# Optimization experiments

Hardware: AMD Instinct MI355X
Metric: run time of the kernel (lower is better)

Reference implementation:

```python
import jax, jax.numpy as jnp
import numpy as np

N_NODES = 100000
N_EDGES = 800000
IN_DIM, HID_DIM, OUT_DIM = 128, 256, 40


def setup_inputs() -> dict:
    key = jax.random.key(0)
    ks = jax.random.split(key, 8)
    x = jax.random.normal(ks[0], (N_NODES, IN_DIM), dtype=jnp.float32)
    edge_index = jax.random.randint(ks[1], (2, N_EDGES), 0, N_NODES, dtype=jnp.int64)
    # PyG SAGEConv params: lin_l (neighbor path, with bias), lin_r (root path, no bias)
    def glorot(k, fan_in, fan_out):
        lim = np.sqrt(6.0 / (fan_in + fan_out)).astype(np.float32)
        return jax.random.uniform(k, (fan_in, fan_out), jnp.float32, -lim, lim)
    W1l = glorot(ks[2], IN_DIM, HID_DIM)
    W1r = glorot(ks[3], IN_DIM, HID_DIM)
    b1 = jnp.zeros((HID_DIM,), jnp.float32)
    W2l = glorot(ks[4], HID_DIM, OUT_DIM)
    W2r = glorot(ks[5], HID_DIM, OUT_DIM)
    b2 = jnp.zeros((OUT_DIM,), jnp.float32)
    return {"x": x, "edge_index": edge_index, "W1l": W1l, "b1": b1, "W1r": W1r,
            "W2l": W2l, "b2": b2, "W2r": W2r}


def _sage_conv(x, src, dst, Wl, b, Wr, n_nodes):
    # mean aggregation of neighbor features: gather x[src], scatter-add to dst, divide by degree
    msg = x[src]                                              # [E, D]
    agg = jax.ops.segment_sum(msg, dst, num_segments=n_nodes)  # [N, D]
    cnt = jax.ops.segment_sum(jnp.ones((src.shape[0],), x.dtype), dst,
                              num_segments=n_nodes)            # [N]
    agg = agg / jnp.maximum(cnt, 1.0)[:, None]
    # out = lin_l(mean_agg) + lin_r(x)  (lin_l carries the bias in PyG)
    return agg @ Wl + b + x @ Wr


def reference(x, edge_index, W1l, b1, W1r, W2l, b2, W2r):
    src, dst = edge_index[0], edge_index[1]
    n = x.shape[0]
    h = _sage_conv(x, src, dst, W1l, b1, W1r, n)
    h = jax.nn.relu(h)
    # F.dropout(training=self.training): identity at inference
    out = _sage_conv(h, src, dst, W2l, b2, W2r, n)
    return out
```

## Files before the change

kernel.cpp:

```cpp
#include <hip/hip_runtime.h>
#include <hip/hip_bf16.h>


#define NN   100000
#define NNP  100096
#define NE   800000
#define NB1  391

typedef unsigned short ushortT;
typedef __attribute__((ext_vector_type(8))) short bf16x8;
typedef __attribute__((ext_vector_type(4))) float f32x4;

__device__ __forceinline__ unsigned short f2b(float f) {
    unsigned u = __float_as_uint(f);
    return (unsigned short)((u + 0x7fffu + ((u >> 16) & 1u)) >> 16);
}
__device__ __forceinline__ float b2f(unsigned short v) {
    return __uint_as_float(((unsigned)v) << 16);
}
__device__ __forceinline__ void llds16(const unsigned short* g, unsigned short* s) {
    __builtin_amdgcn_global_load_lds(
        (const __attribute__((address_space(1))) void*)g,
        (__attribute__((address_space(3))) void*)s, 16, 0, 0);
}

__global__ __launch_bounds__(256) void k_rank(const int* __restrict__ dst,
                                              int* __restrict__ deg,
                                              int* __restrict__ rank) {
    int e = blockIdx.x * 256 + threadIdx.x;
    if (e < NE) rank[e] = atomicAdd(&deg[dst[e]], 1);
}

__global__ __launch_bounds__(256) void k_scan1(const int* __restrict__ deg,
                                               int* __restrict__ rp,
                                               int* __restrict__ bsum) {
    __shared__ int s[256];
    int t = threadIdx.x;
    int i = blockIdx.x * 256 + t;
    int v = (i < NN) ? deg[i] : 0;
    s[t] = v;
    __syncthreads();
    for (int off = 1; off < 256; off <<= 1) {
        int add = (t >= off) ? s[t - off] : 0;
        __syncthreads();
        s[t] += add;
        __syncthreads();
    }
    if (i < NN) rp[i] = s[t] - v;
    if (t == 255) bsum[blockIdx.x] = s[255];
}

__global__ __launch_bounds__(512) void k_scan2(int* __restrict__ bsum) {
    __shared__ int s[512];
    int t = threadIdx.x;
    int v = (t < NB1) ? bsum[t] : 0;
    s[t] = v;
    __syncthreads();
    for (int off = 1; off < 512; off <<= 1) {
        int add = (t >= off) ? s[t - off] : 0;
        __syncthreads();
        s[t] += add;
        __syncthreads();
    }
    if (t < NB1) bsum[t] = s[t] - v;
}

__global__ __launch_bounds__(256) void k_scan3(int* __restrict__ rp,
                                               const int* __restrict__ bsum) {
    int i = blockIdx.x * 256 + threadIdx.x;
    if (i < NN) rp[i] += bsum[blockIdx.x];
    if (i == 0) rp[NN] = NE;
}

__global__ __launch_bounds__(256) void k_fill(const int* __restrict__ src,
                                              const int* __restrict__ dst,
                                              const int* __restrict__ rank,
                                              const int* __restrict__ rp,
                                              int* __restrict__ col) {
    int e = blockIdx.x * 256 + threadIdx.x;
    if (e < NE) col[rp[dst[e]] + rank[e]] = src[e];
}

__global__ __launch_bounds__(256) void k_prep(const float* __restrict__ x,
                                              const float* __restrict__ W1l,
                                              const float* __restrict__ W1r,
                                              const float* __restrict__ W2l,
                                              const float* __restrict__ W2r,
                                              ushortT* __restrict__ Ac,
                                              ushortT* __restrict__ WT1,
                                              ushortT* __restrict__ WT2,
                                              int* __restrict__ deg) {
    int t = blockIdx.x * 256 + threadIdx.x;
    int row = t >> 5, c4 = t & 31;
    float4 v = *(const float4*)&x[(size_t)row * 128 + c4 * 4];
    ushortT* p = Ac + (size_t)row * 256 + 128 + c4 * 4;
    p[0] = f2b(v.x); p[1] = f2b(v.y); p[2] = f2b(v.z); p[3] = f2b(v.w);

    if (t < NN) deg[t] = 0;
    if (t < 65536) {
        int n = t >> 8, k = t & 255;
        float w = (k < 128) ? W1l[(size_t)k * 256 + n] : W1r[(size_t)(k - 128) * 256 + n];
        WT1[t] = f2b(w);
    } else if (t < 65536 + 20480) {
        int j = t - 65536;
        int n = j >> 8, k = j & 255;
        float w = (n < 40) ? W2l[(size_t)k * 40 + n] : W2r[(size_t)k * 40 + (n - 40)];
        WT2[j] = f2b(w);
    }
}

__global__ __launch_bounds__(256) void k_agg1(const int* __restrict__ rp,
                                              const int* __restrict__ col,
                                              ushortT* __restrict__ Ac) {
    int node = blockIdx.x * 4 + (threadIdx.x >> 6);
    int l = threadIdx.x & 63;
    if (node >= NN) return;
    int seg = l >> 4, dl = l & 15;
    int beg = rp[node];
    int deg = rp[node + 1] - beg;
    float a[8] = {0.f, 0.f, 0.f, 0.f, 0.f, 0.f, 0.f, 0.f};
    for (int base = 0; base < deg; base += 64) {
        int cnt = min(64, deg - base);
        int cv = col[beg + base + min(l, cnt - 1)];
        for (int j = 0; j < cnt; j += 8) {
            int e0 = j + seg, e1 = j + 4 + seg;
            int i0 = __shfl(cv, min(e0, cnt - 1));
            int i1 = __shfl(cv, min(e1, cnt - 1));
            bf16x8 v0 = {0, 0, 0, 0, 0, 0, 0, 0};
            bf16x8 v1 = {0, 0, 0, 0, 0, 0, 0, 0};
            if (e0 < cnt) v0 = *(const bf16x8*)(Ac + (size_t)i0 * 256 + 128 + dl * 8);
            if (e1 < cnt) v1 = *(const bf16x8*)(Ac + (size_t)i1 * 256 + 128 + dl * 8);
#pragma unroll
            for (int i = 0; i < 8; ++i)
                a[i] += b2f((unsigned short)v0[i]) + b2f((unsigned short)v1[i]);
        }
    }
#pragma unroll
    for (int i = 0; i < 8; ++i) {
        a[i] += __shfl_xor(a[i], 16);
        a[i] += __shfl_xor(a[i], 32);
    }
    if (seg == 0) {
        float inv = 1.0f / fmaxf((float)deg, 1.0f);
        bf16x8 o;
#pragma unroll
        for (int i = 0; i < 8; ++i) o[i] = (short)f2b(a[i] * inv);
        *(bf16x8*)(Ac + (size_t)node * 256 + dl * 8) = o;
    }
}

__global__ __launch_bounds__(256, 4) void k_gemm1(const ushortT* __restrict__ Ac,
                                                  const ushortT* __restrict__ WT1,
                                                  const float* __restrict__ b1,
                                                  ushortT* __restrict__ h) {
    __shared__ ushortT As[128 * 64];
    __shared__ ushortT Bs[128 * 64];
    const int tid = threadIdx.x, l = tid & 63, wid = tid >> 6;
    const int wm = wid & 1, wn = wid >> 1;
    const int m0 = blockIdx.x * 128;
    const int n0 = blockIdx.y * 128;
    const int q = l >> 4, r = l & 15;
    const int swz = (l & 7) ^ ((l >> 3) & 7);

    f32x4 acc[4][4];
#pragma unroll
    for (int i = 0; i < 4; ++i)
#pragma unroll
        for (int j = 0; j < 4; ++j) acc[i][j] = (f32x4){0.f, 0.f, 0.f, 0.f};

    for (int kt = 0; kt < 256; kt += 64) {
#pragma unroll
        for (int i = 0; i < 4; ++i) {
            int flat = wid * 4 + i;
            int row = flat * 8 + (l >> 3);
            llds16(Ac + (size_t)(m0 + row) * 256 + kt + swz * 8, &As[flat * 512]);
        }
#pragma unroll
        for (int i = 0; i < 4; ++i) {
            int flat = wid * 4 + i;
            int row = flat * 8 + (l >> 3);
            llds16(WT1 + (size_t)(n0 + row) * 256 + kt + swz * 8, &Bs[flat * 512]);
        }
        __syncthreads();
#pragma unroll
        for (int ks = 0; ks < 64; ks += 32) {
            bf16x8 af[4], bfr[4];
            const int c0 = (ks >> 3) + q;
            const int cs = (c0 ^ (r & 7)) * 8;
#pragma unroll
            for (int mt = 0; mt < 4; ++mt)
                af[mt] = *(const bf16x8*)&As[(wm * 64 + mt * 16 + r) * 64 + cs];
#pragma unroll
            for (int nt = 0; nt < 4; ++nt)
                bfr[nt] = *(const bf16x8*)&Bs[(wn * 64 + nt * 16 + r) * 64 + cs];
#pragma unroll
            for (int mt = 0; mt < 4; ++mt)
#pragma unroll
                for (int nt = 0; nt < 4; ++nt)
                    acc[mt][nt] = __builtin_amdgcn_mfma_f32_16x16x32_bf16(
                        af[mt], bfr[nt], acc[mt][nt], 0, 0, 0);
        }
        __syncthreads();
    }
#pragma unroll
    for (int mt = 0; mt < 4; ++mt) {
        int row0 = m0 + wm * 64 + mt * 16 + q * 4;
#pragma unroll
        for (int nt = 0; nt < 4; ++nt) {
            int colb = n0 + wn * 64 + nt * 16 + r;
            float bb = b1[colb];
#pragma unroll
            for (int j = 0; j < 4; ++j) {
                float v = fmaxf(acc[mt][nt][j] + bb, 0.f);
                h[(size_t)(row0 + j) * 256 + colb] = f2b(v);
            }
        }
    }
}

__global__ __launch_bounds__(256, 4) void k_gemm2(const ushortT* __restrict__ h,
                                                  const ushortT* __restrict__ WT2,
                                                  const float* __restrict__ b2,
                                                  ushortT* __restrict__ y2,
                                                  float* __restrict__ t) {
    __shared__ ushortT As[128 * 64];
    __shared__ ushortT Bs[80 * 64];
    const int tid = threadIdx.x, l = tid & 63, wid = tid >> 6;
    const int m0 = blockIdx.x * 128;
    const int q = l >> 4, r = l & 15;
    const int swz = (l & 7) ^ ((l >> 3) & 7);

    f32x4 acc[2][5];
#pragma unroll
    for (int i = 0; i < 2; ++i)
#pragma unroll
        for (int j = 0; j < 5; ++j) acc[i][j] = (f32x4){0.f, 0.f, 0.f, 0.f};

    for (int kt = 0; kt < 256; kt += 64) {
#pragma unroll
        for (int i = 0; i < 4; ++i) {
            int flat = wid * 4 + i;
            int row = flat * 8 + (l >> 3);
            llds16(h + (size_t)(m0 + row) * 256 + kt + swz * 8, &As[flat * 512]);
        }
#pragma unroll
        for (int i = 0; i < 3; ++i) {
            int flat = wid * 3 + i;
            if (flat < 10) {
                int row = flat * 8 + (l >> 3);
                llds16(WT2 + (size_t)row * 256 + kt + swz * 8, &Bs[flat * 512]);
            }
        }
        __syncthreads();
#pragma unroll
        for (int ks = 0; ks < 64; ks += 32) {
            bf16x8 af[2], bfr[5];
            const int c0 = (ks >> 3) + q;
            const int cs = (c0 ^ (r & 7)) * 8;
#pragma unroll
            for (int mt = 0; mt < 2; ++mt)
                af[mt] = *(const bf16x8*)&As[(wid * 32 + mt * 16 + r) * 64 + cs];
#pragma unroll
            for (int nt = 0; nt < 5; ++nt)
                bfr[nt] = *(const bf16x8*)&Bs[(nt * 16 + r) * 64 + cs];
#pragma unroll
            for (int mt = 0; mt < 2; ++mt)
#pragma unroll
                for (int nt = 0; nt < 5; ++nt)
                    acc[mt][nt] = __builtin_amdgcn_mfma_f32_16x16x32_bf16(
                        af[mt], bfr[nt], acc[mt][nt], 0, 0, 0);
        }
        __syncthreads();
    }
#pragma unroll
    for (int mt = 0; mt < 2; ++mt) {
        int row0 = m0 + wid * 32 + mt * 16 + q * 4;
#pragma unroll
        for (int nt = 0; nt < 5; ++nt) {
            int c = nt * 16 + r;
            float bb = (c >= 40) ? b2[c - 40] : 0.f;
#pragma unroll
            for (int j = 0; j < 4; ++j) {
                float v = acc[mt][nt][j];
                if (c < 40)
                    y2[(size_t)(row0 + j) * 40 + c] = f2b(v);
                else
                    t[(size_t)(row0 + j) * 40 + (c - 40)] = v + bb;
            }
        }
    }
}

__global__ __launch_bounds__(256) void k_agg2(const int* __restrict__ rp,
                                              const int* __restrict__ col,
                                              const ushortT* __restrict__ y2,
                                              const float* __restrict__ t,
                                              float* __restrict__ out) {
    int node = blockIdx.x * 4 + (threadIdx.x >> 6);
    int l = threadIdx.x & 63;
    if (node >= NN) return;
    int seg = l >> 4, dl = l & 15;
    int beg = rp[node];
    int deg = rp[node + 1] - beg;
    bool act = dl < 10;
    float a0 = 0.f, a1 = 0.f, a2 = 0.f, a3 = 0.f;
    for (int base = 0; base < deg; base += 64) {
        int cnt = min(64, deg - base);
        int cv = col[beg + base + min(l, cnt - 1)];
        for (int j = 0; j < cnt; j += 8) {
            int e0 = j + seg, e1 = j + 4 + seg;
            int i0 = __shfl(cv, min(e0, cnt - 1));
            int i1 = __shfl(cv, min(e1, cnt - 1));
            ushort4 v0 = {0, 0, 0, 0}, v1 = {0, 0, 0, 0};
            if (e0 < cnt && act) v0 = *(const ushort4*)(y2 + (size_t)i0 * 40 + dl * 4);
            if (e1 < cnt && act) v1 = *(const ushort4*)(y2 + (size_t)i1 * 40 + dl * 4);
            a0 += b2f(v0.x) + b2f(v1.x);
            a1 += b2f(v0.y) + b2f(v1.y);
            a2 += b2f(v0.z) + b2f(v1.z);
            a3 += b2f(v0.w) + b2f(v1.w);
        }
    }
    a0 += __shfl_xor(a0, 16); a0 += __shfl_xor(a0, 32);
    a1 += __shfl_xor(a1, 16); a1 += __shfl_xor(a1, 32);
    a2 += __shfl_xor(a2, 16); a2 += __shfl_xor(a2, 32);
    a3 += __shfl_xor(a3, 16); a3 += __shfl_xor(a3, 32);
    if (seg == 0 && act) {
        float inv = 1.0f / fmaxf((float)deg, 1.0f);
        size_t o = (size_t)node * 40 + dl * 4;
        float4 tv = *(const float4*)&t[o];
        float4 ov;
        ov.x = a0 * inv + tv.x;
        ov.y = a1 * inv + tv.y;
        ov.z = a2 * inv + tv.z;
        ov.w = a3 * inv + tv.w;
        *(float4*)&out[o] = ov;
    }
}

extern "C" void kernel_launch(void* const* d_in, const int* in_sizes, int n_in,
                              void* d_out, int out_size, void* d_ws, size_t ws_size,
                              hipStream_t stream) {
    const float* x   = (const float*)d_in[0];
    const int*   ei  = (const int*)d_in[1];
    const int*   src = ei;
    const int*   dst = ei + NE;
    const float* W1l = (const float*)d_in[2];
    const float* b1  = (const float*)d_in[3];
    const float* W1r = (const float*)d_in[4];
    const float* W2l = (const float*)d_in[5];
    const float* b2  = (const float*)d_in[6];
    const float* W2r = (const float*)d_in[7];
    float* out = (float*)d_out;

    size_t off = 0;
    char* base = (char*)d_ws;
    auto alloc = [&](size_t bytes) -> void* {
        void* p = base + off;
        off += (bytes + 255) & ~(size_t)255;
        return p;
    };
    int*     deg  = (int*)alloc((size_t)NN * 4);
    int*     rp   = (int*)alloc((size_t)(NN + 1) * 4);
    int*     rank = (int*)alloc((size_t)NE * 4);
    int*     bsum = (int*)alloc(512 * 4);
    int*     col  = (int*)alloc((size_t)NE * 4);
    ushortT* Ac   = (ushortT*)alloc((size_t)NNP * 256 * 2);
    ushortT* h    = (ushortT*)alloc((size_t)NNP * 256 * 2);
    ushortT* y2   = (ushortT*)alloc((size_t)NNP * 40 * 2);
    float*   t    = (float*)alloc((size_t)NNP * 40 * 4);
    ushortT* WT1  = (ushortT*)alloc(256 * 256 * 2);
    ushortT* WT2  = (ushortT*)alloc(80 * 256 * 2);

    k_prep<<<(NN * 32) / 256, 256, 0, stream>>>(x, W1l, W1r, W2l, W2r, Ac, WT1, WT2, deg);
    k_rank<<<(NE + 255) / 256, 256, 0, stream>>>(dst, deg, rank);
    k_scan1<<<NB1, 256, 0, stream>>>(deg, rp, bsum);
    k_scan2<<<1, 512, 0, stream>>>(bsum);
    k_scan3<<<NB1, 256, 0, stream>>>(rp, bsum);
    k_fill<<<(NE + 255) / 256, 256, 0, stream>>>(src, dst, rank, rp, col);

    k_agg1<<<(NN + 3) / 4, 256, 0, stream>>>(rp, col, Ac);
    k_gemm1<<<dim3(NNP / 128, 2), 256, 0, stream>>>(Ac, WT1, b1, h);
    k_gemm2<<<NNP / 128, 256, 0, stream>>>(h, WT2, b2, y2, t);
    k_agg2<<<(NN + 3) / 4, 256, 0, stream>>>(rp, col, y2, t, out);
}
```

Baseline: 287.9 us.

## Fuse GEMM1 and GEMM2 via LDS, merge prep/rank, single-pass lookback scan

Fuses the two dense GEMMs into one kernel. Each block computes a 64-row tile of the hidden layer across all 256 columns, keeps the ReLU'd bf16 result in LDS, and multiplies it by WT2 straight away, so the hidden tensor is never written to or read back from global memory. It also merges the prep and rank kernels into one launch, zeroes deg with a memset, and swaps the three-kernel scan for a decoupled-lookback single-pass scan. Risks: each fused block reloads the full WT1 tile, the larger LDS footprint caps occupancy, and the lookback spin-wait assumes earlier blocks get scheduled, which costs time if they are delayed.

```diff
diff --git a/kernel.cpp b/kernel.cpp
--- a/kernel.cpp
+++ b/kernel.cpp
@@ -24,19 +24,50 @@
         (__attribute__((address_space(3))) void*)s, 16, 0, 0);
 }
 
-__global__ __launch_bounds__(256) void k_rank(const int* __restrict__ dst,
-                                              int* __restrict__ deg,
-                                              int* __restrict__ rank) {
-    int e = blockIdx.x * 256 + threadIdx.x;
-    if (e < NE) rank[e] = atomicAdd(&deg[dst[e]], 1);
-}
-
-__global__ __launch_bounds__(256) void k_scan1(const int* __restrict__ deg,
-                                               int* __restrict__ rp,
-                                               int* __restrict__ bsum) {
+__global__ __launch_bounds__(256) void k_prep_rank(
+        const float* __restrict__ x,
+        const float* __restrict__ W1l, const float* __restrict__ W1r,
+        const float* __restrict__ W2l, const float* __restrict__ W2r,
+        ushortT* __restrict__ Ac, ushortT* __restrict__ WT1,
+        ushortT* __restrict__ WT2, int* __restrict__ stat,
+        const int* __restrict__ dst, int* __restrict__ deg,
+        int* __restrict__ rank) {
+    int bid = blockIdx.x;
+    if (bid < 12500) {
+        int t = bid * 256 + threadIdx.x;
+        int row = t >> 5, c4 = t & 31;
+        float4 v = *(const float4*)&x[(size_t)row * 128 + c4 * 4];
+        ushortT* p = Ac + (size_t)row * 256 + 128 + c4 * 4;
+        p[0] = f2b(v.x); p[1] = f2b(v.y); p[2] = f2b(v.z); p[3] = f2b(v.w);
+
+        if (t < 512) stat[t] = 0;
+        if (t < 65536) {
+            int n = t >> 8, k = t & 255;
+            float w = (k < 128) ? W1l[(size_t)k * 256 + n]
+                                : W1r[(size_t)(k - 128) * 256 + n];
+            WT1[t] = f2b(w);
+        } else if (t < 65536 + 20480) {
+            int j = t - 65536;
+            int n = j >> 8, k = j & 255;
+            float w = (n < 40) ? W2l[(size_t)k * 40 + n]
+                               : W2r[(size_t)k * 40 + (n - 40)];
+            WT2[j] = f2b(w);
+        }
+    } else {
+        int e = (bid - 12500) * 256 + threadIdx.x;
+        if (e < NE) rank[e] = atomicAdd(&deg[dst[e]], 1);
+    }
+}
+
+__global__ __launch_bounds__(256) void k_scan(const int* __restrict__ deg,
+                                              int* __restrict__ rp,
+                                              int* __restrict__ aggv,
+                                              int* __restrict__ prefv,
+                                              int* __restrict__ stat) {
     __shared__ int s[256];
-    int t = threadIdx.x;
-    int i = blockIdx.x * 256 + t;
+    __shared__ int sprefix;
+    int t = threadIdx.x, b = blockIdx.x;
+    int i = b * 256 + t;
     int v = (i < NN) ? deg[i] : 0;
     s[t] = v;
     __syncthreads();
@@ -46,30 +77,36 @@
         s[t] += add;
         __syncthreads();
     }
-    if (i < NN) rp[i] = s[t] - v;
-    if (t == 255) bsum[blockIdx.x] = s[255];
-}
-
-__global__ __launch_bounds__(512) void k_scan2(int* __restrict__ bsum) {
-    __shared__ int s[512];
-    int t = threadIdx.x;
-    int v = (t < NB1) ? bsum[t] : 0;
-    s[t] = v;
+    int total = s[255];
+    if (t == 0) {
+        if (b == 0) {
+            __hip_atomic_store(&prefv[0], total, __ATOMIC_RELEASE, __HIP_MEMORY_SCOPE_AGENT);
+            __hip_atomic_store(&stat[0], 2, __ATOMIC_RELEASE, __HIP_MEMORY_SCOPE_AGENT);
+            sprefix = 0;
+        } else {
+            __hip_atomic_store(&aggv[b], total, __ATOMIC_RELEASE, __HIP_MEMORY_SCOPE_AGENT);
+            __hip_atomic_store(&stat[b], 1, __ATOMIC_RELEASE, __HIP_MEMORY_SCOPE_AGENT);
+            int run = 0, j = b - 1;
+            while (true) {
+                int sj;
+                do {
+                    sj = __hip_atomic_load(&stat[j], __ATOMIC_ACQUIRE, __HIP_MEMORY_SCOPE_AGENT);
+                } while (sj == 0);
+                if (sj == 2) {
+                    run += __hip_atomic_load(&prefv[j], __ATOMIC_ACQUIRE, __HIP_MEMORY_SCOPE_AGENT);
+                    break;
+                }
+                run += __hip_atomic_load(&aggv[j], __ATOMIC_ACQUIRE, __HIP_MEMORY_SCOPE_AGENT);
+                --j;
+            }
+            __hip_atomic_store(&prefv[b], run + total, __ATOMIC_RELEASE, __HIP_MEMORY_SCOPE_AGENT);
+            __hip_atomic_store(&stat[b], 2, __ATOMIC_RELEASE, __HIP_MEMORY_SCOPE_AGENT);
+            sprefix = run;
+        }
+    }
     __syncthreads();
-    for (int off = 1; off < 512; off <<= 1) {
-        int add = (t >= off) ? s[t - off] : 0;
-        __syncthreads();
-        s[t] += add;
-        __syncthreads();
-    }
-    if (t < NB1) bsum[t] = s[t] - v;
-}
-
-__global__ __launch_bounds__(256) void k_scan3(int* __restrict__ rp,
-                                               const int* __restrict__ bsum) {
-    int i = blockIdx.x * 256 + threadIdx.x;
-    if (i < NN) rp[i] += bsum[blockIdx.x];
-    if (i == 0) rp[NN] = NE;
+    if (i < NN) rp[i] = sprefix + s[t] - v;
+    if (i == NN - 1) rp[NN] = NE;
 }
 
 __global__ __launch_bounds__(256) void k_fill(const int* __restrict__ src,
@@ -79,34 +116,6 @@
                                               int* __restrict__ col) {
     int e = blockIdx.x * 256 + threadIdx.x;
     if (e < NE) col[rp[dst[e]] + rank[e]] = src[e];
-}
-
-__global__ __launch_bounds__(256) void k_prep(const float* __restrict__ x,
-                                              const float* __restrict__ W1l,
-                                              const float* __restrict__ W1r,
-                                              const float* __restrict__ W2l,
-                                              const float* __restrict__ W2r,
-                                              ushortT* __restrict__ Ac,
-                                              ushortT* __restrict__ WT1,
-                                              ushortT* __restrict__ WT2,
-                                              int* __restrict__ deg) {
-    int t = blockIdx.x * 256 + threadIdx.x;
-    int row = t >> 5, c4 = t & 31;
-    float4 v = *(const float4*)&x[(size_t)row * 128 + c4 * 4];
-    ushortT* p = Ac + (size_t)row * 256 + 128 + c4 * 4;
-    p[0] = f2b(v.x); p[1] = f2b(v.y); p[2] = f2b(v.z); p[3] = f2b(v.w);
-
-    if (t < NN) deg[t] = 0;
-    if (t < 65536) {
-        int n = t >> 8, k = t & 255;
-        float w = (k < 128) ? W1l[(size_t)k * 256 + n] : W1r[(size_t)(k - 128) * 256 + n];
-        WT1[t] = f2b(w);
-    } else if (t < 65536 + 20480) {
-        int j = t - 65536;
-        int n = j >> 8, k = j & 255;
-        float w = (n < 40) ? W2l[(size_t)k * 40 + n] : W2r[(size_t)k * 40 + (n - 40)];
-        WT2[j] = f2b(w);
-    }
 }
 
 __global__ __launch_bounds__(256) void k_agg1(const int* __restrict__ rp,
@@ -149,16 +158,16 @@
     }
 }
 
-__global__ __launch_bounds__(256, 4) void k_gemm1(const ushortT* __restrict__ Ac,
-                                                  const ushortT* __restrict__ WT1,
-                                                  const float* __restrict__ b1,
-                                                  ushortT* __restrict__ h) {
-    __shared__ ushortT As[128 * 64];
-    __shared__ ushortT Bs[128 * 64];
+#define HSP 264
+__global__ __launch_bounds__(256, 3) void k_fused(
+        const ushortT* __restrict__ Ac, const ushortT* __restrict__ WT1,
+        const float* __restrict__ b1, const ushortT* __restrict__ WT2,
+        const float* __restrict__ b2, ushortT* __restrict__ y2,
+        float* __restrict__ t) {
+    __shared__ ushortT As[64 * 64];
+    __shared__ ushortT Bs[64 * HSP];
     const int tid = threadIdx.x, l = tid & 63, wid = tid >> 6;
-    const int wm = wid & 1, wn = wid >> 1;
-    const int m0 = blockIdx.x * 128;
-    const int n0 = blockIdx.y * 128;
+    const int m0 = blockIdx.x * 64;
     const int q = l >> 4, r = l & 15;
     const int swz = (l & 7) ^ ((l >> 3) & 7);
 
@@ -170,29 +179,28 @@
 
     for (int kt = 0; kt < 256; kt += 64) {
 #pragma unroll
-        for (int i = 0; i < 4; ++i) {
-            int flat = wid * 4 + i;
+        for (int i = 0; i < 2; ++i) {
+            int flat = wid * 2 + i;
             int row = flat * 8 + (l >> 3);
             llds16(Ac + (size_t)(m0 + row) * 256 + kt + swz * 8, &As[flat * 512]);
         }
 #pragma unroll
-        for (int i = 0; i < 4; ++i) {
-            int flat = wid * 4 + i;
+        for (int i = 0; i < 8; ++i) {
+            int flat = wid * 8 + i;
             int row = flat * 8 + (l >> 3);
-            llds16(WT1 + (size_t)(n0 + row) * 256 + kt + swz * 8, &Bs[flat * 512]);
+            llds16(WT1 + (size_t)row * 256 + kt + swz * 8, &Bs[flat * 512]);
         }
         __syncthreads();
 #pragma unroll
         for (int ks = 0; ks < 64; ks += 32) {
             bf16x8 af[4], bfr[4];
-            const int c0 = (ks >> 3) + q;
-            const int cs = (c0 ^ (r & 7)) * 8;
+            const int cs = (((ks >> 3) + q) ^ (r & 7)) * 8;
 #pragma unroll
             for (int mt = 0; mt < 4; ++mt)
-                af[mt] = *(const bf16x8*)&As[(wm * 64 + mt * 16 + r) * 64 + cs];
+                af[mt] = *(const bf16x8*)&As[(mt * 16 + r) * 64 + cs];
 #pragma unroll
             for (int nt = 0; nt < 4; ++nt)
-                bfr[nt] = *(const bf16x8*)&Bs[(wn * 64 + nt * 16 + r) * 64 + cs];
+                bfr[nt] = *(const bf16x8*)&Bs[(wid * 64 + nt * 16 + r) * 64 + cs];
 #pragma unroll
             for (int mt = 0; mt < 4; ++mt)
 #pragma unroll
@@ -203,85 +211,54 @@
         __syncthreads();
     }
 #pragma unroll
-    for (int mt = 0; mt < 4; ++mt) {
-        int row0 = m0 + wm * 64 + mt * 16 + q * 4;
-#pragma unroll
-        for (int nt = 0; nt < 4; ++nt) {
-            int colb = n0 + wn * 64 + nt * 16 + r;
-            float bb = b1[colb];
+    for (int nt = 0; nt < 4; ++nt) {
+        int colb = wid * 64 + nt * 16 + r;
+        float bb = b1[colb];
+#pragma unroll
+        for (int mt = 0; mt < 4; ++mt) {
+            int rowb = mt * 16 + q * 4;
+#pragma unroll
+            for (int j = 0; j < 4; ++j)
+                Bs[(rowb + j) * HSP + colb] = f2b(fmaxf(acc[mt][nt][j] + bb, 0.f));
+        }
+    }
+    __syncthreads();
+
+    f32x4 acc2[2][4];
+#pragma unroll
+    for (int i = 0; i < 2; ++i)
+#pragma unroll
+        for (int j = 0; j < 4; ++j) acc2[i][j] = (f32x4){0.f, 0.f, 0.f, 0.f};
+#pragma unroll
+    for (int kk = 0; kk < 256; kk += 32) {
+        bf16x8 af[4];
+#pragma unroll
+        for (int mt = 0; mt < 4; ++mt)
+            af[mt] = *(const bf16x8*)&Bs[(mt * 16 + r) * HSP + kk + q * 8];
+#pragma unroll
+        for (int cc = 0; cc < 2; ++cc) {
+            int ct = wid + cc * 4;
+            if (ct < 5) {
+                bf16x8 bq = *(const bf16x8*)(WT2 + (size_t)(ct * 16 + r) * 256 + kk + q * 8);
+#pragma unroll
+                for (int mt = 0; mt < 4; ++mt)
+                    acc2[cc][mt] = __builtin_amdgcn_mfma_f32_16x16x32_bf16(
+                        af[mt], bq, acc2[cc][mt], 0, 0, 0);
+            }
+        }
+    }
+#pragma unroll
+    for (int cc = 0; cc < 2; ++cc) {
+        int ct = wid + cc * 4;
+        if (ct >= 5) continue;
+        int c = ct * 16 + r;
+        float bb = (c >= 40) ? b2[c - 40] : 0.f;
+#pragma unroll
+        for (int mt = 0; mt < 4; ++mt) {
+            int row0 = m0 + mt * 16 + q * 4;
 #pragma unroll
             for (int j = 0; j < 4; ++j) {
-                float v = fmaxf(acc[mt][nt][j] + bb, 0.f);
-                h[(size_t)(row0 + j) * 256 + colb] = f2b(v);
-            }
-        }
-    }
-}
-
-__global__ __launch_bounds__(256, 4) void k_gemm2(const ushortT* __restrict__ h,
-                                                  const ushortT* __restrict__ WT2,
-                                                  const float* __restrict__ b2,
-                                                  ushortT* __restrict__ y2,
-                                                  float* __restrict__ t) {
-    __shared__ ushortT As[128 * 64];
-    __shared__ ushortT Bs[80 * 64];
-    const int tid = threadIdx.x, l = tid & 63, wid = tid >> 6;
-    const int m0 = blockIdx.x * 128;
-    const int q = l >> 4, r = l & 15;
-    const int swz = (l & 7) ^ ((l >> 3) & 7);
-
-    f32x4 acc[2][5];
-#pragma unroll
-    for (int i = 0; i < 2; ++i)
-#pragma unroll
-        for (int j = 0; j < 5; ++j) acc[i][j] = (f32x4){0.f, 0.f, 0.f, 0.f};
-
-    for (int kt = 0; kt < 256; kt += 64) {
-#pragma unroll
-        for (int i = 0; i < 4; ++i) {
-            int flat = wid * 4 + i;
-            int row = flat * 8 + (l >> 3);
-            llds16(h + (size_t)(m0 + row) * 256 + kt + swz * 8, &As[flat * 512]);
-        }
-#pragma unroll
-        for (int i = 0; i < 3; ++i) {
-            int flat = wid * 3 + i;
-            if (flat < 10) {
-                int row = flat * 8 + (l >> 3);
-                llds16(WT2 + (size_t)row * 256 + kt + swz * 8, &Bs[flat * 512]);
-            }
-        }
-        __syncthreads();
-#pragma unroll
-        for (int ks = 0; ks < 64; ks += 32) {
-            bf16x8 af[2], bfr[5];
-            const int c0 = (ks >> 3) + q;
-            const int cs = (c0 ^ (r & 7)) * 8;
-#pragma unroll
-            for (int mt = 0; mt < 2; ++mt)
-                af[mt] = *(const bf16x8*)&As[(wid * 32 + mt * 16 + r) * 64 + cs];
-#pragma unroll
-            for (int nt = 0; nt < 5; ++nt)
-                bfr[nt] = *(const bf16x8*)&Bs[(nt * 16 + r) * 64 + cs];
-#pragma unroll
-            for (int mt = 0; mt < 2; ++mt)
-#pragma unroll
-                for (int nt = 0; nt < 5; ++nt)
-                    acc[mt][nt] = __builtin_amdgcn_mfma_f32_16x16x32_bf16(
-                        af[mt], bfr[nt], acc[mt][nt], 0, 0, 0);
-        }
-        __syncthreads();
-    }
-#pragma unroll
-    for (int mt = 0; mt < 2; ++mt) {
-        int row0 = m0 + wid * 32 + mt * 16 + q * 4;
-#pragma unroll
-        for (int nt = 0; nt < 5; ++nt) {
-            int c = nt * 16 + r;
-            float bb = (c >= 40) ? b2[c - 40] : 0.f;
-#pragma unroll
-            for (int j = 0; j < 4; ++j) {
-                float v = acc[mt][nt][j];
+                float v = acc2[cc][mt][j];
                 if (c < 40)
                     y2[(size_t)(row0 + j) * 40 + c] = f2b(v);
                 else
@@ -359,27 +336,25 @@
         off += (bytes + 255) & ~(size_t)255;
         return p;
     };
-    int*     deg  = (int*)alloc((size_t)NN * 4);
-    int*     rp   = (int*)alloc((size_t)(NN + 1) * 4);
-    int*     rank = (int*)alloc((size_t)NE * 4);
-    int*     bsum = (int*)alloc(512 * 4);
-    int*     col  = (int*)alloc((size_t)NE * 4);
-    ushortT* Ac   = (ushortT*)alloc((size_t)NNP * 256 * 2);
-    ushortT* h    = (ushortT*)alloc((size_t)NNP * 256 * 2);
-    ushortT* y2   = (ushortT*)alloc((size_t)NNP * 40 * 2);
-    float*   t    = (float*)alloc((size_t)NNP * 40 * 4);
-    ushortT* WT1  = (ushortT*)alloc(256 * 256 * 2);
-    ushortT* WT2  = (ushortT*)alloc(80 * 256 * 2);
-
-    k_prep<<<(NN * 32) / 256, 256, 0, stream>>>(x, W1l, W1r, W2l, W2r, Ac, WT1, WT2, deg);
-    k_rank<<<(NE + 255) / 256, 256, 0, stream>>>(dst, deg, rank);
-    k_scan1<<<NB1, 256, 0, stream>>>(deg, rp, bsum);
-    k_scan2<<<1, 512, 0, stream>>>(bsum);
-    k_scan3<<<NB1, 256, 0, stream>>>(rp, bsum);
+    int*     deg   = (int*)alloc((size_t)NN * 4);
+    int*     rp    = (int*)alloc((size_t)(NN + 1) * 4);
+    int*     rank  = (int*)alloc((size_t)NE * 4);
+    int*     col   = (int*)alloc((size_t)NE * 4);
+    int*     aggv  = (int*)alloc(512 * 4);
+    int*     prefv = (int*)alloc(512 * 4);
+    int*     stat  = (int*)alloc(512 * 4);
+    ushortT* Ac    = (ushortT*)alloc((size_t)NNP * 256 * 2);
+    ushortT* y2    = (ushortT*)alloc((size_t)NNP * 40 * 2);
+    float*   t     = (float*)alloc((size_t)NNP * 40 * 4);
+    ushortT* WT1   = (ushortT*)alloc(256 * 256 * 2);
+    ushortT* WT2   = (ushortT*)alloc(80 * 256 * 2);
+
+    hipMemsetAsync(deg, 0, (size_t)NN * 4, stream);
+    k_prep_rank<<<15625, 256, 0, stream>>>(x, W1l, W1r, W2l, W2r, Ac, WT1, WT2,
+                                           stat, dst, deg, rank);
+    k_scan<<<NB1, 256, 0, stream>>>(deg, rp, aggv, prefv, stat);
     k_fill<<<(NE + 255) / 256, 256, 0, stream>>>(src, dst, rank, rp, col);
-
     k_agg1<<<(NN + 3) / 4, 256, 0, stream>>>(rp, col, Ac);
-    k_gemm1<<<dim3(NNP / 128, 2), 256, 0, stream>>>(Ac, WT1, b1, h);
-    k_gemm2<<<NNP / 128, 256, 0, stream>>>(h, WT2, b2, y2, t);
+    k_fused<<<NNP / 64, 256, 0, stream>>>(Ac, WT1, b1, WT2, b2, y2, t);
     k_agg2<<<(NN + 3) / 4, 256, 0, stream>>>(rp, col, y2, t, out);
 }
```

Measured after the change: 461.3 us. 60.2% more time.
